# Performance work log

Measured on AMD Instinct MI355X. Metric: run time of the kernel, lower is better.

Reference implementation:

```python
import jax, jax.numpy as jnp
import numpy as np


def setup_inputs() -> dict:
    key = jax.random.key(0)
    k1, k2 = jax.random.split(key)
    B, H, W, E = 8, 32, 32, 256   # latent grid (NHWC layout, as in vector_quantize)
    N_E = 16384                   # codebook size
    x = jax.random.normal(k1, (B, H, W, E), dtype=jnp.float32)
    codebook = jax.random.normal(k2, (N_E, E), dtype=jnp.float32)
    return {"x": x, "codebook": codebook}


def reference(x, codebook):
    # d[b,h,w,k] = ||x[b,h,w] - codebook[k]||^2 (expanded form, as in source)
    x_sq = jnp.sum(x * x, axis=-1, keepdims=True)            # [B,H,W,1]
    cb_sq = jnp.sum(codebook * codebook, axis=1)              # [N_E]
    cross = jnp.einsum('bhwe,ke->bhwk', x, codebook)          # [B,H,W,N_E]
    d = x_sq + cb_sq - 2.0 * cross
    indices = jnp.argmin(d, axis=-1)                          # [B,H,W]
    x_q = jnp.take(codebook, indices, axis=0)                 # one-hot @ codebook == row gather
    # straight-through / ReplaceGrad: forward value is x_q, gradient flows to x
    return x + jax.lax.stop_gradient(x_q - x)
```

## Files before the change

### kernel.cpp

```cpp
#include <hip/hip_runtime.h>
#include <stdint.h>

#define M_PIX 8192
#define N_CB  16384
#define KD    256

typedef float f32x4 __attribute__((ext_vector_type(4)));
typedef int   i32x4 __attribute__((ext_vector_type(4)));
typedef int   i32x8 __attribute__((ext_vector_type(8)));
typedef unsigned long long ull;

#define OFF_CF8  (0ULL)
#define OFF_XF8  (4ULL << 20)
#define OFF_CBSQ (6ULL << 20)
#define OFF_SLOT (7ULL << 20)
#define WS_REQ   (15ULL << 20)

__device__ __forceinline__ unsigned int fkey(float s) {
  unsigned int f = __float_as_uint(s);
  return f ^ ((unsigned int)(((int)f) >> 31) | 0x80000000u);
}
__device__ __forceinline__ unsigned char f2e4m3(float v) {
  float av = fminf(fabsf(v), 448.0f);
  const unsigned s = (__float_as_uint(v) >> 24) & 0x80u;
  unsigned m;
  if (av >= 0.015625f) {
    unsigned u = __float_as_uint(av);
    u += 0x7FFFFu + ((u >> 20) & 1u);
    m = (((u >> 23) - 120u) << 3) | ((u >> 20) & 7u);
  } else {
    m = (unsigned)(int)rintf(av * 512.0f);
  }
  return (unsigned char)(s | m);
}
__device__ __forceinline__ void gl_lds16(const unsigned char* g, char* l) {
  __builtin_amdgcn_global_load_lds(
      (const __attribute__((address_space(1))) unsigned int*)(const void*)g,
      (__attribute__((address_space(3))) unsigned int*)(void*)l,
      16, 0, 0);
}
__device__ __forceinline__ void ins2f(float k, float& v1, float& v2) {
  v2 = fminf(v2, fmaxf(v1, k));
  v1 = fminf(v1, k);
}
__device__ __forceinline__ i32x8 ld32(const char* p, int addr) {
  const i32x4 lo = *(const i32x4*)(const void*)(p + addr);
  const i32x4 hi = *(const i32x4*)(const void*)(p + (addr ^ 16));
  return (i32x8){lo.x, lo.y, lo.z, lo.w, hi.x, hi.y, hi.z, hi.w};
}

__global__ __launch_bounds__(256) void prep_kernel(
    const float* __restrict__ x, const float* __restrict__ cb,
    unsigned char* __restrict__ Cf8, unsigned char* __restrict__ Xf8,
    float* __restrict__ cbsq) {
  const int wid = threadIdx.x >> 6, lane = threadIdx.x & 63;
  const int row = blockIdx.x * 4 + wid;
  const bool isCb = (row < N_CB);
  const int rowL = isCb ? row : row - N_CB;
  const float* src = (isCb ? cb : x) + (size_t)rowL * KD;
  const float4 v = ((const float4*)src)[lane];
  uchar4 pk;
  pk.x = f2e4m3(v.x); pk.y = f2e4m3(v.y); pk.z = f2e4m3(v.z); pk.w = f2e4m3(v.w);
  *(uchar4*)(void*)((isCb ? Cf8 : Xf8) + (size_t)rowL * KD + lane * 4) = pk;
  if (isCb) {
    float ss = v.x*v.x + v.y*v.y + v.z*v.z + v.w*v.w;
    #pragma unroll
    for (int off = 32; off > 0; off >>= 1) ss += __shfl_xor(ss, off);
    if (lane == 0) cbsq[rowL] = ss;
  }
}


__global__ __launch_bounds__(256, 3) void gemm_top2_kernel(
    const unsigned char* __restrict__ Xf8, const unsigned char* __restrict__ Cf8,
    const float* __restrict__ cbsq, float2* __restrict__ slots) {
  __shared__ __align__(16) char smem[36864];
  char* A_s = smem;
  char* B_s = smem + 16384;
  float* v1p = (float*)smem;
  float* v2p = (float*)(smem + 18432);

  const int tid = threadIdx.x;
  const int wid = tid >> 6, lane = tid & 63;
  const int wy = wid >> 1, wx = wid & 1;
  const int q = lane >> 4, c = lane & 15;

  const int bx = blockIdx.x & 7, bg = blockIdx.x >> 3;
  const int mt = bg >> 4;
  const int nt = bx * 16 + (bg & 15);
  const int m0 = mt * 128, n0 = nt * 128;

  const int swz = (c & 7) << 4;
  int aaddr[4], baddr[4];
  #pragma unroll
  for (int i = 0; i < 4; i++) {
    aaddr[i] = (((wy * 64 + i * 16 + c) * 128) + q * 32) ^ swz;
    baddr[i] = (((wx * 64 + i * 16 + c) * 128) + q * 32) ^ swz;
  }

  const f32x4 zf = {0.f, 0.f, 0.f, 0.f};
  f32x4 acc[4][4];
  #pragma unroll
  for (int i = 0; i < 4; i++)
    #pragma unroll
    for (int j = 0; j < 4; j++) acc[i][j] = zf;

  const int srow8 = lane >> 3;
  const int sgb = ((lane & 7) ^ srow8) * 16;

  #pragma unroll
  for (int hk = 0; hk < 2; hk++) {
    if (hk) __syncthreads();
    #pragma unroll
    for (int j = 0; j < 4; j++) {
      const int chunk = j * 4 + wid;
      const int row = chunk * 8 + srow8;
      const int gb = sgb + hk * 128;
      gl_lds16(Xf8 + (size_t)(m0 + row) * KD + gb, A_s + chunk * 1024);
      gl_lds16(Cf8 + (size_t)(n0 + row) * KD + gb, B_s + chunk * 1024);
    }
    __syncthreads();
    i32x8 bfr[4];
    #pragma unroll
    for (int ni = 0; ni < 4; ni++)
      bfr[ni] = ld32(B_s, baddr[ni]);
    #pragma unroll
    for (int mi = 0; mi < 4; mi++) {
      const i32x8 af = ld32(A_s, aaddr[mi]);
      #pragma unroll
      for (int ni = 0; ni < 4; ni++)
        acc[mi][ni] = __builtin_amdgcn_mfma_scale_f32_16x16x128_f8f6f4(
            af, bfr[ni], acc[mi][ni], 0, 0,
            0, 0x7F7F7F7F,
            0, 0x7F7F7F7F);
    }
  }
  __syncthreads();

  float cs[4]; unsigned colp[4];
  #pragma unroll
  for (int ni = 0; ni < 4; ni++) {
    colp[ni] = wx * 64 + ni * 16 + c;
    cs[ni] = cbsq[n0 + colp[ni]];
  }
  const float FINF = __uint_as_float(0x7F800000u);

  #pragma unroll
  for (int mi = 0; mi < 4; mi++) {
    #pragma unroll
    for (int r = 0; r < 4; r++) {
      float v1 = FINF, v2 = FINF;
      #pragma unroll
      for (int ni = 0; ni < 4; ni++) {
        const float s = fmaf(-2.f, acc[mi][ni][r], cs[ni]);
        ins2f(__uint_as_float((__float_as_uint(s) & 0xFFFFFF80u) | colp[ni]),
              v1, v2);
      }
      const int row = wy * 64 + mi * 16 + q * 4 + r;
      const int slot = wx * 16 + c;
      v1p[row * 36 + slot] = v1;
      v2p[row * 36 + slot] = v2;
    }
  }
  __syncthreads();

  {
    const int srow = tid >> 1, half = tid & 1;
    float v1 = FINF, v2 = FINF;
    #pragma unroll
    for (int jj = 0; jj < 2; jj++) {
      const float4 a = *(const float4*)(const void*)(v1p + srow * 36 + half * 16 + jj * 8);
      const float4 a2 = *(const float4*)(const void*)(v1p + srow * 36 + half * 16 + jj * 8 + 4);
      const float4 b = *(const float4*)(const void*)(v2p + srow * 36 + half * 16 + jj * 8);
      const float4 b2 = *(const float4*)(const void*)(v2p + srow * 36 + half * 16 + jj * 8 + 4);
      ins2f(a.x, v1, v2);  ins2f(a.y, v1, v2);
      ins2f(a.z, v1, v2);  ins2f(a.w, v1, v2);
      ins2f(a2.x, v1, v2); ins2f(a2.y, v1, v2);
      ins2f(a2.z, v1, v2); ins2f(a2.w, v1, v2);
      ins2f(b.x, v1, v2);  ins2f(b.y, v1, v2);
      ins2f(b.z, v1, v2);  ins2f(b.w, v1, v2);
      ins2f(b2.x, v1, v2); ins2f(b2.y, v1, v2);
      ins2f(b2.z, v1, v2); ins2f(b2.w, v1, v2);
    }
    const float b1 = __shfl_xor(v1, 1), b2 = __shfl_xor(v2, 1);
    const float hi = fmaxf(v1, b1);
    v1 = fminf(v1, b1);
    v2 = fminf(fminf(v2, b2), hi);
    if (!half)
      slots[(size_t)nt * M_PIX + m0 + srow] = make_float2(v1, v2);
  }
}

__global__ __launch_bounds__(256) void reduce_rescore_gather(
    const float* __restrict__ x, const float* __restrict__ cb,
    const float* __restrict__ cbsq, const float2* __restrict__ slots,
    float* __restrict__ out) {
  const int wid = threadIdx.x >> 6, lane = threadIdx.x & 63;
  const int pixel = blockIdx.x * 4 + wid;

  const float2 sA = slots[(size_t)lane * M_PIX + pixel];
  const float2 sB = slots[(size_t)(64 + lane) * M_PIX + pixel];
  const float sc[4] = {sA.x, sA.y, sB.x, sB.y};
  float mn = fminf(fminf(sc[0], sc[1]), fminf(sc[2], sc[3]));
  #pragma unroll
  for (int off = 1; off < 64; off <<= 1) mn = fminf(mn, __shfl_xor(mn, off));
  const float thr = mn + 10.0f;

  const float4 xv = ((const float4*)x)[(size_t)pixel * 64 + lane];
  ull best = ~0ULL;
  #pragma unroll
  for (int j = 0; j < 4; j++) {
    ull mask = __ballot(sc[j] < thr);
    while (mask) {
      const int src = (int)__ffsll((long long)mask) - 1;
      mask &= mask - 1;
      const float val = __shfl(sc[j], src);
      const unsigned ij = (unsigned)(((j >> 1) * 64 + src) * 128) +
                          (__float_as_uint(val) & 127u);
      const float4 cv = ((const float4*)cb)[(size_t)ij * 64 + lane];
      float d = xv.x*cv.x + xv.y*cv.y + xv.z*cv.z + xv.w*cv.w;
      #pragma unroll
      for (int off = 1; off < 64; off <<= 1) d += __shfl_xor(d, off);
      const float sv = fmaf(-2.f, d, cbsq[ij]);
      const ull k = ((ull)fkey(sv) << 32) | ij;
      best = k < best ? k : best;
    }
  }
  const unsigned w = (unsigned)best;
  ((float4*)out)[(size_t)pixel * 64 + lane] = ((const float4*)cb)[(size_t)w * 64 + lane];
}

__global__ __launch_bounds__(256) void fallback_kernel(
    const float* __restrict__ x, const float* __restrict__ cb,
    float* __restrict__ out) {
  __shared__ float xs[256];
  __shared__ unsigned long long keys[4];
  __shared__ int widx;
  const int p = blockIdx.x;
  const int tid = threadIdx.x, wid = tid >> 6, lane = tid & 63;
  xs[tid] = x[(size_t)p * KD + tid];
  __syncthreads();
  const float4 xv = ((const float4*)xs)[lane];
  float bestS = 3.4e38f; int bestI = 0;
  for (int k = wid; k < N_CB; k += 4) {
    const float4 cv = ((const float4*)cb)[(size_t)k * 64 + lane];
    float t = cv.x*(cv.x - 2.f*xv.x) + cv.y*(cv.y - 2.f*xv.y)
            + cv.z*(cv.z - 2.f*xv.z) + cv.w*(cv.w - 2.f*xv.w);
    #pragma unroll
    for (int off = 1; off < 64; off <<= 1) t += __shfl_xor(t, off);
    if (t < bestS) { bestS = t; bestI = k; }
  }
  if (lane == 0)
    keys[wid] = ((unsigned long long)fkey(bestS) << 32) | (unsigned int)bestI;
  __syncthreads();
  if (tid == 0) {
    unsigned long long m = keys[0];
    for (int i = 1; i < 4; i++) if (keys[i] < m) m = keys[i];
    widx = (int)(unsigned int)(m & 0xFFFFFFFFULL);
  }
  __syncthreads();
  out[(size_t)p * KD + tid] = cb[(size_t)widx * KD + tid];
}

extern "C" void kernel_launch(void* const* d_in, const int* in_sizes, int n_in,
                              void* d_out, int out_size, void* d_ws, size_t ws_size,
                              hipStream_t stream) {
  const float* x  = (const float*)d_in[0];
  const float* cb = (const float*)d_in[1];
  float* out = (float*)d_out;

  if (ws_size < WS_REQ) {
    fallback_kernel<<<M_PIX, 256, 0, stream>>>(x, cb, out);
    return;
  }

  char* ws = (char*)d_ws;
  unsigned char* Cf8 = (unsigned char*)(ws + OFF_CF8);
  unsigned char* Xf8 = (unsigned char*)(ws + OFF_XF8);
  float* cbsq        = (float*)(ws + OFF_CBSQ);
  float2* slots      = (float2*)(ws + OFF_SLOT);

  prep_kernel<<<(N_CB + M_PIX) / 4, 256, 0, stream>>>(x, cb, Cf8, Xf8, cbsq);
  gemm_top2_kernel<<<M_PIX, 256, 0, stream>>>(Xf8, Cf8, cbsq, slots);
  reduce_rescore_gather<<<M_PIX / 4, 256, 0, stream>>>(x, cb, cbsq, slots, out);
}
```

Baseline: 144.9 us.

## Issue both K-half loads upfront into separate LDS buffers and overlap with compute

```diff
diff --git a/kernel.cpp b/kernel.cpp
--- a/kernel.cpp
+++ b/kernel.cpp
@@ -71,12 +71,27 @@
 }
 
 
+#define COMPUTE_HALF(HOFF)                                                    \
+  do {                                                                        \
+    i32x8 bfr[4];                                                             \
+    _Pragma("unroll")                                                         \
+    for (int ni = 0; ni < 4; ni++)                                            \
+      bfr[ni] = ld32(smem, baddr[ni] + (HOFF));                               \
+    _Pragma("unroll")                                                         \
+    for (int mi = 0; mi < 4; mi++) {                                          \
+      const i32x8 af = ld32(smem, aaddr[mi] + (HOFF));                        \
+      _Pragma("unroll")                                                       \
+      for (int ni = 0; ni < 4; ni++)                                          \
+        acc[mi][ni] = __builtin_amdgcn_mfma_scale_f32_16x16x128_f8f6f4(       \
+            af, bfr[ni], acc[mi][ni], 0, 0,                                   \
+            0, 0x7F7F7F7F, 0, 0x7F7F7F7F);                                    \
+    }                                                                         \
+  } while (0)
+
 __global__ __launch_bounds__(256, 3) void gemm_top2_kernel(
     const unsigned char* __restrict__ Xf8, const unsigned char* __restrict__ Cf8,
     const float* __restrict__ cbsq, float2* __restrict__ slots) {
-  __shared__ __align__(16) char smem[36864];
-  char* A_s = smem;
-  char* B_s = smem + 16384;
+  __shared__ __align__(16) char smem[65536];
   float* v1p = (float*)smem;
   float* v2p = (float*)(smem + 18432);
 
@@ -94,8 +109,8 @@
   int aaddr[4], baddr[4];
   #pragma unroll
   for (int i = 0; i < 4; i++) {
-    aaddr[i] = (((wy * 64 + i * 16 + c) * 128) + q * 32) ^ swz;
-    baddr[i] = (((wx * 64 + i * 16 + c) * 128) + q * 32) ^ swz;
+    aaddr[i] = ((((wy * 64 + i * 16 + c) * 128) + q * 32) ^ swz);
+    baddr[i] = ((((wx * 64 + i * 16 + c) * 128) + q * 32) ^ swz) + 16384;
   }
 
   const f32x4 zf = {0.f, 0.f, 0.f, 0.f};
@@ -110,31 +125,34 @@
 
   #pragma unroll
   for (int hk = 0; hk < 2; hk++) {
-    if (hk) __syncthreads();
+    char* As = smem + hk * 32768;
+    char* Bs = As + 16384;
     #pragma unroll
     for (int j = 0; j < 4; j++) {
       const int chunk = j * 4 + wid;
       const int row = chunk * 8 + srow8;
       const int gb = sgb + hk * 128;
-      gl_lds16(Xf8 + (size_t)(m0 + row) * KD + gb, A_s + chunk * 1024);
-      gl_lds16(Cf8 + (size_t)(n0 + row) * KD + gb, B_s + chunk * 1024);
+      gl_lds16(Xf8 + (size_t)(m0 + row) * KD + gb, As + chunk * 1024);
+      gl_lds16(Cf8 + (size_t)(n0 + row) * KD + gb, Bs + chunk * 1024);
     }
-    __syncthreads();
-    i32x8 bfr[4];
-    #pragma unroll
-    for (int ni = 0; ni < 4; ni++)
-      bfr[ni] = ld32(B_s, baddr[ni]);
-    #pragma unroll
-    for (int mi = 0; mi < 4; mi++) {
-      const i32x8 af = ld32(A_s, aaddr[mi]);
-      #pragma unroll
-      for (int ni = 0; ni < 4; ni++)
-        acc[mi][ni] = __builtin_amdgcn_mfma_scale_f32_16x16x128_f8f6f4(
-            af, bfr[ni], acc[mi][ni], 0, 0,
-            0, 0x7F7F7F7F,
-            0, 0x7F7F7F7F);
-    }
-  }
+    __builtin_amdgcn_sched_barrier(0);
+  }
+
+  asm volatile("s_waitcnt vmcnt(8)" ::: "memory");
+  __builtin_amdgcn_s_barrier();
+  asm volatile("" ::: "memory");
+  __builtin_amdgcn_sched_barrier(0);
+
+  COMPUTE_HALF(0);
+
+  __builtin_amdgcn_sched_barrier(0);
+  asm volatile("s_waitcnt vmcnt(0)" ::: "memory");
+  __builtin_amdgcn_s_barrier();
+  asm volatile("" ::: "memory");
+  __builtin_amdgcn_sched_barrier(0);
+
+  COMPUTE_HALF(32768);
+
   __syncthreads();
 
   float cs[4]; unsigned colp[4];
```

Measured after the change: 153.9 us. +6.2%, slower.

## Load MFMA operands directly from global memory instead of staging through LDS

Applied to the files above, without the earlier changes.

```diff
diff --git a/kernel.cpp b/kernel.cpp
--- a/kernel.cpp
+++ b/kernel.cpp
@@ -33,19 +33,13 @@
   }
   return (unsigned char)(s | m);
 }
-__device__ __forceinline__ void gl_lds16(const unsigned char* g, char* l) {
-  __builtin_amdgcn_global_load_lds(
-      (const __attribute__((address_space(1))) unsigned int*)(const void*)g,
-      (__attribute__((address_space(3))) unsigned int*)(void*)l,
-      16, 0, 0);
-}
 __device__ __forceinline__ void ins2f(float k, float& v1, float& v2) {
   v2 = fminf(v2, fmaxf(v1, k));
   v1 = fminf(v1, k);
 }
-__device__ __forceinline__ i32x8 ld32(const char* p, int addr) {
-  const i32x4 lo = *(const i32x4*)(const void*)(p + addr);
-  const i32x4 hi = *(const i32x4*)(const void*)(p + (addr ^ 16));
+__device__ __forceinline__ i32x8 gload32(const unsigned char* p) {
+  const i32x4 lo = *(const i32x4*)(const void*)p;
+  const i32x4 hi = *(const i32x4*)(const void*)(p + 16);
   return (i32x8){lo.x, lo.y, lo.z, lo.w, hi.x, hi.y, hi.z, hi.w};
 }
 
@@ -74,11 +68,9 @@
 __global__ __launch_bounds__(256, 3) void gemm_top2_kernel(
     const unsigned char* __restrict__ Xf8, const unsigned char* __restrict__ Cf8,
     const float* __restrict__ cbsq, float2* __restrict__ slots) {
-  __shared__ __align__(16) char smem[36864];
-  char* A_s = smem;
-  char* B_s = smem + 16384;
-  float* v1p = (float*)smem;
-  float* v2p = (float*)(smem + 18432);
+  __shared__ __align__(16) float smem[9216];
+  float* v1p = smem;
+  float* v2p = smem + 4608;
 
   const int tid = threadIdx.x;
   const int wid = tid >> 6, lane = tid & 63;
@@ -90,13 +82,8 @@
   const int nt = bx * 16 + (bg & 15);
   const int m0 = mt * 128, n0 = nt * 128;
 
-  const int swz = (c & 7) << 4;
-  int aaddr[4], baddr[4];
-  #pragma unroll
-  for (int i = 0; i < 4; i++) {
-    aaddr[i] = (((wy * 64 + i * 16 + c) * 128) + q * 32) ^ swz;
-    baddr[i] = (((wx * 64 + i * 16 + c) * 128) + q * 32) ^ swz;
-  }
+  const unsigned char* Abase = Xf8 + (size_t)(m0 + wy * 64 + c) * KD + q * 32;
+  const unsigned char* Bbase = Cf8 + (size_t)(n0 + wx * 64 + c) * KD + q * 32;
 
   const f32x4 zf = {0.f, 0.f, 0.f, 0.f};
   f32x4 acc[4][4];
@@ -105,37 +92,23 @@
     #pragma unroll
     for (int j = 0; j < 4; j++) acc[i][j] = zf;
 
-  const int srow8 = lane >> 3;
-  const int sgb = ((lane & 7) ^ srow8) * 16;
-
   #pragma unroll
   for (int hk = 0; hk < 2; hk++) {
-    if (hk) __syncthreads();
-    #pragma unroll
-    for (int j = 0; j < 4; j++) {
-      const int chunk = j * 4 + wid;
-      const int row = chunk * 8 + srow8;
-      const int gb = sgb + hk * 128;
-      gl_lds16(Xf8 + (size_t)(m0 + row) * KD + gb, A_s + chunk * 1024);
-      gl_lds16(Cf8 + (size_t)(n0 + row) * KD + gb, B_s + chunk * 1024);
-    }
-    __syncthreads();
-    i32x8 bfr[4];
-    #pragma unroll
-    for (int ni = 0; ni < 4; ni++)
-      bfr[ni] = ld32(B_s, baddr[ni]);
-    #pragma unroll
-    for (int mi = 0; mi < 4; mi++) {
-      const i32x8 af = ld32(A_s, aaddr[mi]);
+    const int ho = hk * 128;
+    i32x8 bf[4], af[4];
+    #pragma unroll
+    for (int ni = 0; ni < 4; ni++) bf[ni] = gload32(Bbase + ni * 16 * KD + ho);
+    #pragma unroll
+    for (int mi = 0; mi < 4; mi++) af[mi] = gload32(Abase + mi * 16 * KD + ho);
+    #pragma unroll
+    for (int mi = 0; mi < 4; mi++)
       #pragma unroll
       for (int ni = 0; ni < 4; ni++)
         acc[mi][ni] = __builtin_amdgcn_mfma_scale_f32_16x16x128_f8f6f4(
-            af, bfr[ni], acc[mi][ni], 0, 0,
+            af[mi], bf[ni], acc[mi][ni], 0, 0,
             0, 0x7F7F7F7F,
             0, 0x7F7F7F7F);
-    }
-  }
-  __syncthreads();
+  }
 
   float cs[4]; unsigned colp[4];
   #pragma unroll
@@ -143,19 +116,21 @@
     colp[ni] = wx * 64 + ni * 16 + c;
     cs[ni] = cbsq[n0 + colp[ni]];
   }
-  const float FINF = __uint_as_float(0x7F800000u);
 
   #pragma unroll
   for (int mi = 0; mi < 4; mi++) {
     #pragma unroll
     for (int r = 0; r < 4; r++) {
-      float v1 = FINF, v2 = FINF;
+      float k[4];
       #pragma unroll
       for (int ni = 0; ni < 4; ni++) {
         const float s = fmaf(-2.f, acc[mi][ni][r], cs[ni]);
-        ins2f(__uint_as_float((__float_as_uint(s) & 0xFFFFFF80u) | colp[ni]),
-              v1, v2);
+        k[ni] = __uint_as_float((__float_as_uint(s) & 0xFFFFFF80u) | colp[ni]);
       }
+      const float m1 = fminf(k[0], k[1]), M1 = fmaxf(k[0], k[1]);
+      const float m2 = fminf(k[2], k[3]), M2 = fmaxf(k[2], k[3]);
+      const float v1 = fminf(m1, m2);
+      const float v2 = fminf(fmaxf(m1, m2), fminf(M1, M2));
       const int row = wy * 64 + mi * 16 + q * 4 + r;
       const int slot = wx * 16 + c;
       v1p[row * 36 + slot] = v1;
@@ -165,6 +140,7 @@
   __syncthreads();
 
   {
+    const float FINF = __uint_as_float(0x7F800000u);
     const int srow = tid >> 1, half = tid & 1;
     float v1 = FINF, v2 = FINF;
     #pragma unroll
```

After: 209.6 us. +44.7%, slower.
